# Performance work log

Measured on AMD Instinct MI355X. Metric: run time of the kernel, lower is better.

The kernel has to match this reference:

```python
import jax, jax.numpy as jnp
import numpy as np
from math import sqrt

P_DROP = 0.2  # dropout_rate

def setup_inputs() -> dict:
    key = jax.random.key(0)
    ks = jax.random.split(key, 5)
    B, Cin, H, W = 32, 128, 64, 64
    Cout, kh, kw = 256, 3, 3
    k = sqrt(1.0 / (Cin * kh * kw))  # He-style init std from module
    x = jax.random.normal(ks[0], (B, Cin, H, W), dtype=jnp.float32)
    weight = jax.random.normal(ks[1], (Cout, Cin, kh, kw), dtype=jnp.float32) * k
    bias = jax.random.normal(ks[2], (Cout,), dtype=jnp.float32) * k
    # uniforms used for torch.rand(...) > p per batch element ('w' mode draws fresh masks per sample)
    u_w = jax.random.uniform(ks[3], (B, Cout, Cin, kh, kw), dtype=jnp.float32)
    u_b = jax.random.uniform(ks[4], (B, Cout), dtype=jnp.float32)
    return {"x": x, "weight": weight, "bias": bias, "u_w": u_w, "u_b": u_b}

def reference(x, weight, bias, u_w, u_b):
    # 'w' mode: per-sample dropped-out weight/bias, conv per sample -> vmapped batched conv.
    # Note: mask is (rand > p) with NO 1/(1-p) rescaling, matching the torch code.
    w_mask = (u_w > P_DROP).astype(weight.dtype)          # [B,O,I,kh,kw]
    b_mask = (u_b > P_DROP).astype(bias.dtype)            # [B,O]
    w_per = weight[None] * w_mask                          # [B,O,I,kh,kw]
    b_per = bias[None] * b_mask                            # [B,O]

    def conv_one(xi, wi):  # xi: [Cin,H,W], wi: [O,I,kh,kw]
        return jax.lax.conv_general_dilated(
            xi[None], wi,
            window_strides=(1, 1),
            padding=((1, 1), (1, 1)),
            dimension_numbers=("NCHW", "OIHW", "NCHW"),
        )[0]

    y = jax.vmap(conv_one)(x, w_per)                       # [B,O,H,W]
    return y + b_per[:, :, None, None]
```

## Files before the change

### kernel.cpp

```cpp
#include <hip/hip_runtime.h>
#include <cstdint>
#include <cstddef>

#define CIN   128
#define COUT  256
#define HW    64
#define NSP   4096
#define KTOT  1152
#define BATCH 32
#define PDROP 0.2f
#define LDT   40

__device__ __forceinline__ unsigned short f2bf(float f) {
    unsigned int u = __builtin_bit_cast(unsigned int, f);
    u += 0x7fffu + ((u >> 16) & 1u);
    return (unsigned short)(u >> 16);
}

__device__ __align__(16) unsigned short g_zeros[64] = {0};

__device__ __forceinline__ void gl_lds16(const unsigned short* g, unsigned short* l) {
    __builtin_amdgcn_global_load_lds(
        (const __attribute__((address_space(1))) unsigned int*)g,
        (__attribute__((address_space(3))) unsigned int*)l,
        16, 0, 0);
}

__global__ __launch_bounds__(256) void prepass(
        const float* __restrict__ weight, const float* __restrict__ u_w,
        const float* __restrict__ x,
        unsigned short* __restrict__ wt, unsigned short* __restrict__ xt)
{
    __shared__ unsigned int shp[64 * 65];
    unsigned short* sh16 = reinterpret_cast<unsigned short*>(shp);
    const int t256 = threadIdx.x;

    if (blockIdx.x < 4096) {
        const int half = t256 >> 7;
        const int i    = t256 & 127;
        const int bo   = blockIdx.x * 2 + half;
        const int o    = bo & (COUT - 1);
        unsigned short* tile = sh16 + half * KTOT;
        const float* wsrc = weight + (size_t)o  * KTOT + i * 9;
        const float* usrc = u_w    + (size_t)bo * KTOT + i * 9;
        float wv9[9], uv9[9];
        #pragma unroll
        for (int r = 0; r < 9; ++r) { wv9[r] = wsrc[r]; uv9[r] = usrc[r]; }
        #pragma unroll
        for (int r = 0; r < 9; ++r)
            tile[r * CIN + i] = f2bf((uv9[r] > PDROP) ? wv9[r] : 0.f);
        __syncthreads();
        const uint4* src = reinterpret_cast<const uint4*>(tile);
        uint4* dst = reinterpret_cast<uint4*>(wt + (size_t)bo * KTOT);
        dst[i] = src[i];
        if (i < 16) dst[128 + i] = src[128 + i];
    } else {
        const int bidx = blockIdx.x - 4096;
        const int b    = bidx >> 6;
        const int hw0  = (bidx & 63) * 64;
        const int ib   = t256 >> 4;
        const int hw4  = (t256 & 15) * 4;
        #pragma unroll
        for (int j = 0; j < 4; ++j) {
            const int p = ib + 16 * j;
            const float4 v0 = *reinterpret_cast<const float4*>(
                x + ((size_t)(b * CIN + 2 * p)) * NSP + hw0 + hw4);
            const float4 v1 = *reinterpret_cast<const float4*>(
                x + ((size_t)(b * CIN + 2 * p + 1)) * NSP + hw0 + hw4);
            const float e0[4] = {v0.x, v0.y, v0.z, v0.w};
            const float e1[4] = {v1.x, v1.y, v1.z, v1.w};
            #pragma unroll
            for (int c = 0; c < 4; ++c) {
                const unsigned int val =
                    (unsigned int)f2bf(e0[c]) | ((unsigned int)f2bf(e1[c]) << 16);
                shp[(hw4 + c) * 65 + p] = val;
            }
        }
        __syncthreads();
        #pragma unroll
        for (int j = 0; j < 4; ++j) {
            const int idx  = j * 256 + t256;
            const int row  = idx >> 4;
            const int part = idx & 15;
            uint4 v;
            v.x = shp[row * 65 + part * 4 + 0];
            v.y = shp[row * 65 + part * 4 + 1];
            v.z = shp[row * 65 + part * 4 + 2];
            v.w = shp[row * 65 + part * 4 + 3];
            *reinterpret_cast<uint4*>(
                xt + ((size_t)(b * NSP + hw0 + row)) * CIN + part * 8) = v;
        }
    }
}

__global__ __launch_bounds__(256, 2) void conv_v5(
        const unsigned short* __restrict__ wt,
        const unsigned short* __restrict__ xt,
        const float* __restrict__ bias, const float* __restrict__ u_b,
        float* __restrict__ out)
{
    using frag  = __attribute__((ext_vector_type(8))) short;
    using f32x4 = __attribute__((ext_vector_type(4))) float;

    __shared__ unsigned short Xs[4 * 66 * 64];
    __shared__ unsigned short As[2][128 * 64];

    const int tid  = threadIdx.x;
    const int lane = tid & 63;
    const int q    = lane >> 4;
    const int l15  = lane & 15;
    const int wv   = tid >> 6;
    const int wm   = (wv >> 1) * 64;
    const int wn   = (wv & 1) * 64;
    const int wnrow = wn >> 6;

    const int f   = blockIdx.x + 32 * blockIdx.y + 64 * blockIdx.z;
    const int wid = (f & 7) * 256 + (f >> 3);
    const int b   = wid >> 6;
    const int m0  = ((wid >> 5) & 1) * 128;
    const int n0  = (wid & 31) * 128;
    const int ph0 = n0 >> 6;

    const unsigned short* wtb = wt + (size_t)(b * COUT + m0) * KTOT;
    const unsigned short* xtb = xt + (size_t)b * NSP * CIN;

    const int r8 = lane >> 3;
    const int p8 = lane & 7;
    const int cx = p8 ^ r8;
    const unsigned short* gA[4];
    #pragma unroll
    for (int j = 0; j < 4; ++j) {
        const int row = wv * 32 + j * 8 + r8;
        gA[j] = wtb + (size_t)row * KTOT + cx * 8;
    }

    const int kcl = (lane & 7) ^ ((1 + (lane >> 3)) & 7);
    const int xsrc_lane = (lane >> 3) * CIN + kcl * 8;
    const int hhx = ph0 - 1 + wv;
    const bool vrow = ((unsigned)hhx < 64u);
    unsigned short* const xdst = &Xs[(wv * 66 + 1) * 64];

    const int l7 = l15 & 7;
    const int physk0 = q ^ l7;
    const int physk1 = (4 + q) ^ l7;
    const int a_base = (wm + l15) * 64;
    int xoff[4];
    #pragma unroll
    for (int ni = 0; ni < 4; ++ni) xoff[ni] = (ni * 16 + l15 + 1) * 64;
    int xr[3][2];
    #pragma unroll
    for (int dxi = 0; dxi < 3; ++dxi)
        #pragma unroll
        for (int ki = 0; ki < 2; ++ki)
            xr[dxi][ki] = ((ki * 4 + q) ^ ((l15 + dxi) & 7)) * 8;

    f32x4 acc[4][4];
    #pragma unroll
    for (int i = 0; i < 4; ++i)
        #pragma unroll
        for (int j = 0; j < 4; ++j)
            acc[i][j] = (f32x4){0.f, 0.f, 0.f, 0.f};

    {
        const int cell = tid >> 5;
        const int rr   = cell >> 1;
        const int cc   = (cell & 1) ? 65 : 0;
        *reinterpret_cast<unsigned int*>(
            &Xs[(rr * 66 + cc) * 64 + (tid & 31) * 2]) = 0u;
    }

    auto stage_a = [&](int k0, int buf) {
        #pragma unroll
        for (int j = 0; j < 4; ++j)
            gl_lds16(gA[j] + k0, &As[buf][(wv * 32 + j * 8) * 64]);
    };
    auto stage_x = [&](int i0) {
        const unsigned short* sx = vrow
            ? xtb + (size_t)hhx * HW * CIN + i0 + xsrc_lane
            : g_zeros;
        #pragma unroll
        for (int g = 0; g < 8; ++g)
            gl_lds16(vrow ? (sx + g * 8 * CIN) : sx, xdst + g * 512);
    };

    stage_a(0, 0);
    stage_x(0);

    #pragma unroll
    for (int it = 0; it < 18; ++it) {
        const int tap = it % 9;
        const int cur = it & 1;

        if (it == 9) stage_x(64);

        if (it < 17) {
            const int nit = it + 1;
            stage_a((nit % 9) * 128 + (nit / 9) * 64, nit & 1);
        }

        if (it == 0)      asm volatile("s_waitcnt vmcnt(4) lgkmcnt(0)" ::: "memory");
        else if (it < 17) asm volatile("s_waitcnt vmcnt(4)" ::: "memory");
        else              asm volatile("s_waitcnt vmcnt(0)" ::: "memory");
        __builtin_amdgcn_s_barrier();

        const int dy  = tap / 3 - 1;
        const int dx  = tap - 3 * (tap / 3) - 1;
        const int dxi = dx + 1;
        const int cb  = (wnrow + dy + 1) * 4224 + dx * 64;

        __builtin_amdgcn_s_setprio(1);
        #pragma unroll
        for (int ki = 0; ki < 2; ++ki) {
            const int pk = ki ? physk1 : physk0;
            frag af[4], bfr[4];
            #pragma unroll
            for (int mi = 0; mi < 4; ++mi)
                af[mi] = *reinterpret_cast<const frag*>(
                    &As[cur][a_base + mi * 1024 + pk * 8]);
            #pragma unroll
            for (int ni = 0; ni < 4; ++ni)
                bfr[ni] = *reinterpret_cast<const frag*>(
                    &Xs[cb + xoff[ni] + xr[dxi][ki]]);
            #pragma unroll
            for (int mi = 0; mi < 4; ++mi)
                #pragma unroll
                for (int ni = 0; ni < 4; ++ni)
                    acc[mi][ni] = __builtin_amdgcn_mfma_f32_16x16x32_bf16(
                        af[mi], bfr[ni], acc[mi][ni], 0, 0, 0);
        }
        __builtin_amdgcn_s_setprio(0);

        if (it < 17) __builtin_amdgcn_s_barrier();
    }

    float* ob = out + (size_t)b * COUT * NSP;
    #pragma unroll
    for (int mi = 0; mi < 4; ++mi) {
        #pragma unroll
        for (int rg = 0; rg < 4; ++rg) {
            const int o  = m0 + wm + mi * 16 + q * 4 + rg;
            const float bvv = (u_b[b * COUT + o] > PDROP) ? bias[o] : 0.f;
            float* orow = ob + (size_t)o * NSP + n0 + wn + l15;
            #pragma unroll
            for (int ni = 0; ni < 4; ++ni)
                orow[ni * 16] = acc[mi][ni][rg] + bvv;
        }
    }
}

template<bool USE_WS>
__global__ __launch_bounds__(256) void conv_fb(
        const float* __restrict__ x, const float* __restrict__ weight,
        const float* __restrict__ bias, const float* __restrict__ u_w,
        const float* __restrict__ u_b, const unsigned short* __restrict__ wt,
        float* __restrict__ out)
{
    using frag  = __attribute__((ext_vector_type(8))) short;
    using f32x4 = __attribute__((ext_vector_type(4))) float;

    __shared__ unsigned short As[128 * LDT];
    __shared__ unsigned short Bs[128 * LDT];

    const int tid  = threadIdx.x;
    const int lane = tid & 63;
    const int q    = lane >> 4;
    const int l15  = lane & 15;
    const int wv   = tid >> 6;
    const int wm   = (wv >> 1) * 64;
    const int wn   = (wv & 1) * 64;

    const int b  = blockIdx.z;
    const int m0 = blockIdx.y * 128;
    const int n0 = blockIdx.x * 128;

    const int arow = tid >> 1;
    const int acol = (tid & 1) * 16;
    const int pn = tid & 127;
    const int kh = (tid >> 7) * 16;
    const int p  = n0 + pn;
    const int ph = p >> 6;
    const int pw = p & 63;

    const float* xb = x + (size_t)b * CIN * NSP;

    f32x4 acc[4][4];
    #pragma unroll
    for (int i = 0; i < 4; ++i)
        #pragma unroll
        for (int j = 0; j < 4; ++j)
            acc[i][j] = (f32x4){0.f, 0.f, 0.f, 0.f};

    const int a_rd = (wm + l15) * LDT + q * 8;
    const int b_rd = (wn + l15) * LDT + q * 8;

    for (int s = 0; s < 36; ++s) {
        const int r  = s >> 2;
        const int i0 = (s & 3) * 32;
        const int k0 = s * 32;

        uint4 av0, av1;
        float aw[16], au[16];
        if (USE_WS) {
            const uint4* src = reinterpret_cast<const uint4*>(
                wt + ((size_t)(b * COUT + m0 + arow)) * KTOT + k0 + acol);
            av0 = src[0];
            av1 = src[1];
        } else {
            const float* wsrc = weight + (size_t)(m0 + arow) * KTOT;
            const float* usrc = u_w + (size_t)(b * COUT + m0 + arow) * KTOT;
            #pragma unroll
            for (int ii = 0; ii < 16; ++ii) {
                const int kk = (i0 + acol + ii) * 9 + r;
                aw[ii] = wsrc[kk];
                au[ii] = usrc[kk];
            }
        }

        const int hh = ph + (r / 3) - 1;
        const int ww = pw + (r % 3) - 1;
        float bx[16];
        #pragma unroll
        for (int j = 0; j < 16; ++j) bx[j] = 0.f;
        if (((unsigned)hh < 64u) && ((unsigned)ww < 64u)) {
            const float* xsrc = xb + (size_t)(i0 + kh) * NSP + hh * HW + ww;
            #pragma unroll
            for (int j = 0; j < 16; ++j) bx[j] = xsrc[(size_t)j * NSP];
        }

        __syncthreads();

        if (USE_WS) {
            uint4* d = reinterpret_cast<uint4*>(&As[arow * LDT + acol]);
            d[0] = av0; d[1] = av1;
        } else {
            union { unsigned short u16[16]; uint4 v[2]; } tu;
            #pragma unroll
            for (int ii = 0; ii < 16; ++ii)
                tu.u16[ii] = f2bf((au[ii] > PDROP) ? aw[ii] : 0.f);
            uint4* d = reinterpret_cast<uint4*>(&As[arow * LDT + acol]);
            d[0] = tu.v[0]; d[1] = tu.v[1];
        }
        {
            union { unsigned short u16[16]; uint4 v[2]; } tu;
            #pragma unroll
            for (int j = 0; j < 16; ++j) tu.u16[j] = f2bf(bx[j]);
            uint4* d = reinterpret_cast<uint4*>(&Bs[pn * LDT + kh]);
            d[0] = tu.v[0]; d[1] = tu.v[1];
        }

        __syncthreads();

        frag af[4], bfr[4];
        #pragma unroll
        for (int mi = 0; mi < 4; ++mi)
            af[mi] = *reinterpret_cast<const frag*>(&As[a_rd + mi * 16 * LDT]);
        #pragma unroll
        for (int ni = 0; ni < 4; ++ni)
            bfr[ni] = *reinterpret_cast<const frag*>(&Bs[b_rd + ni * 16 * LDT]);
        #pragma unroll
        for (int mi = 0; mi < 4; ++mi)
            #pragma unroll
            for (int ni = 0; ni < 4; ++ni)
                acc[mi][ni] = __builtin_amdgcn_mfma_f32_16x16x32_bf16(
                    af[mi], bfr[ni], acc[mi][ni], 0, 0, 0);
    }

    float* ob = out + (size_t)b * COUT * NSP;
    #pragma unroll
    for (int mi = 0; mi < 4; ++mi) {
        #pragma unroll
        for (int rg = 0; rg < 4; ++rg) {
            const int o = m0 + wm + mi * 16 + q * 4 + rg;
            const float bvv = (u_b[b * COUT + o] > PDROP) ? bias[o] : 0.f;
            float* orow = ob + (size_t)o * NSP + n0 + wn + l15;
            #pragma unroll
            for (int ni = 0; ni < 4; ++ni)
                orow[ni * 16] = acc[mi][ni][rg] + bvv;
        }
    }
}

extern "C" void kernel_launch(void* const* d_in, const int* in_sizes, int n_in,
                              void* d_out, int out_size, void* d_ws, size_t ws_size,
                              hipStream_t stream)
{
    const float* x      = (const float*)d_in[0];
    const float* weight = (const float*)d_in[1];
    const float* bias   = (const float*)d_in[2];
    const float* u_w    = (const float*)d_in[3];
    const float* u_b    = (const float*)d_in[4];
    float* out = (float*)d_out;

    const size_t wt_bytes = (size_t)BATCH * COUT * KTOT * sizeof(unsigned short);
    const size_t xt_bytes = (size_t)BATCH * NSP * CIN * sizeof(unsigned short);
    dim3 grid(NSP / 128, COUT / 128, BATCH);

    if (ws_size >= wt_bytes + xt_bytes) {
        unsigned short* wtp = (unsigned short*)d_ws;
        unsigned short* xtp = (unsigned short*)((char*)d_ws + wt_bytes);
        prepass<<<4096 + 2048, 256, 0, stream>>>(weight, u_w, x, wtp, xtp);
        conv_v5<<<grid, 256, 0, stream>>>(wtp, xtp, bias, u_b, out);
    } else if (ws_size >= wt_bytes) {
        unsigned short* wtp = (unsigned short*)d_ws;
        prepass<<<4096, 256, 0, stream>>>(weight, u_w, x, wtp, nullptr);
        conv_fb<true><<<grid, 256, 0, stream>>>(x, weight, bias, u_w, u_b, wtp, out);
    } else {
        conv_fb<false><<<grid, 256, 0, stream>>>(x, weight, bias, u_w, u_b, nullptr, out);
    }
}
```

Baseline: 299.0 us.

## Load weight fragments directly from global into registers, dropping LDS A staging

The weight (A) operand no longer goes through a double-buffered LDS tile. Each lane now loads its MFMA fragments straight from global memory into registers, prefetching one k-step ahead, and the per-iteration barriers go away. Freeing the 32KB of A shared memory lets the launch bound rise to three blocks per SM. The cost is that each wave re-fetches weight rows from global/L2 instead of sharing them through LDS, and those loads are uncoalesced 16-byte per-lane reads whose latency is hidden only by a single-stage register prefetch.

```diff
diff --git a/kernel.cpp b/kernel.cpp
--- a/kernel.cpp
+++ b/kernel.cpp
@@ -93,7 +93,7 @@
     }
 }
 
-__global__ __launch_bounds__(256, 2) void conv_v5(
+__global__ __launch_bounds__(256, 3) void conv_v6(
         const unsigned short* __restrict__ wt,
         const unsigned short* __restrict__ xt,
         const float* __restrict__ bias, const float* __restrict__ u_b,
@@ -103,7 +103,6 @@
     using f32x4 = __attribute__((ext_vector_type(4))) float;
 
     __shared__ unsigned short Xs[4 * 66 * 64];
-    __shared__ unsigned short As[2][128 * 64];
 
     const int tid  = threadIdx.x;
     const int lane = tid & 63;
@@ -124,15 +123,11 @@
     const unsigned short* wtb = wt + (size_t)(b * COUT + m0) * KTOT;
     const unsigned short* xtb = xt + (size_t)b * NSP * CIN;
 
-    const int r8 = lane >> 3;
-    const int p8 = lane & 7;
-    const int cx = p8 ^ r8;
-    const unsigned short* gA[4];
-    #pragma unroll
-    for (int j = 0; j < 4; ++j) {
-        const int row = wv * 32 + j * 8 + r8;
-        gA[j] = wtb + (size_t)row * KTOT + cx * 8;
-    }
+    const char* gAr[4];
+    #pragma unroll
+    for (int mi = 0; mi < 4; ++mi)
+        gAr[mi] = reinterpret_cast<const char*>(
+            wtb + (size_t)(wm + mi * 16 + l15) * KTOT + q * 8);
 
     const int kcl = (lane & 7) ^ ((1 + (lane >> 3)) & 7);
     const int xsrc_lane = (lane >> 3) * CIN + kcl * 8;
@@ -140,10 +135,6 @@
     const bool vrow = ((unsigned)hhx < 64u);
     unsigned short* const xdst = &Xs[(wv * 66 + 1) * 64];
 
-    const int l7 = l15 & 7;
-    const int physk0 = q ^ l7;
-    const int physk1 = (4 + q) ^ l7;
-    const int a_base = (wm + l15) * 64;
     int xoff[4];
     #pragma unroll
     for (int ni = 0; ni < 4; ++ni) xoff[ni] = (ni * 16 + l15 + 1) * 64;
@@ -169,11 +160,6 @@
             &Xs[(rr * 66 + cc) * 64 + (tid & 31) * 2]) = 0u;
     }
 
-    auto stage_a = [&](int k0, int buf) {
-        #pragma unroll
-        for (int j = 0; j < 4; ++j)
-            gl_lds16(gA[j] + k0, &As[buf][(wv * 32 + j * 8) * 64]);
-    };
     auto stage_x = [&](int i0) {
         const unsigned short* sx = vrow
             ? xtb + (size_t)hhx * HW * CIN + i0 + xsrc_lane
@@ -183,54 +169,50 @@
             gl_lds16(vrow ? (sx + g * 8 * CIN) : sx, xdst + g * 512);
     };
 
-    stage_a(0, 0);
-    stage_x(0);
-
-    #pragma unroll
-    for (int it = 0; it < 18; ++it) {
-        const int tap = it % 9;
-        const int cur = it & 1;
-
-        if (it == 9) stage_x(64);
-
-        if (it < 17) {
-            const int nit = it + 1;
-            stage_a((nit % 9) * 128 + (nit / 9) * 64, nit & 1);
-        }
-
-        if (it == 0)      asm volatile("s_waitcnt vmcnt(4) lgkmcnt(0)" ::: "memory");
-        else if (it < 17) asm volatile("s_waitcnt vmcnt(4)" ::: "memory");
-        else              asm volatile("s_waitcnt vmcnt(0)" ::: "memory");
-        __builtin_amdgcn_s_barrier();
-
-        const int dy  = tap / 3 - 1;
-        const int dx  = tap - 3 * (tap / 3) - 1;
-        const int dxi = dx + 1;
-        const int cb  = (wnrow + dy + 1) * 4224 + dx * 64;
-
-        __builtin_amdgcn_s_setprio(1);
-        #pragma unroll
-        for (int ki = 0; ki < 2; ++ki) {
-            const int pk = ki ? physk1 : physk0;
-            frag af[4], bfr[4];
-            #pragma unroll
-            for (int mi = 0; mi < 4; ++mi)
-                af[mi] = *reinterpret_cast<const frag*>(
-                    &As[cur][a_base + mi * 1024 + pk * 8]);
+    #pragma unroll
+    for (int s2 = 0; s2 < 2; ++s2) {
+        const int i0 = s2 * 64;
+
+        if (s2) __syncthreads();
+        stage_x(i0);
+        __syncthreads();
+
+        frag afr[2][4];
+        #pragma unroll
+        for (int mi = 0; mi < 4; ++mi)
+            afr[0][mi] = *reinterpret_cast<const frag*>(gAr[mi] + (i0 * 2));
+
+        #pragma unroll
+        for (int p = 0; p < 18; ++p) {
+            const int cur = p & 1;
+            if (p + 1 < 18) {
+                const int koff = (((p + 1) >> 1) * 128 + i0 + ((p + 1) & 1) * 32) * 2;
+                #pragma unroll
+                for (int mi = 0; mi < 4; ++mi)
+                    afr[cur ^ 1][mi] = *reinterpret_cast<const frag*>(gAr[mi] + koff);
+            }
+            const int tap = p >> 1;
+            const int ki  = p & 1;
+            const int dy  = tap / 3 - 1;
+            const int dx  = tap - 3 * (tap / 3) - 1;
+            const int dxi = dx + 1;
+            const int cb  = (wnrow + dy + 1) * 4224 + dx * 64;
+
+            frag bfr[4];
             #pragma unroll
             for (int ni = 0; ni < 4; ++ni)
                 bfr[ni] = *reinterpret_cast<const frag*>(
                     &Xs[cb + xoff[ni] + xr[dxi][ki]]);
+
+            __builtin_amdgcn_s_setprio(1);
             #pragma unroll
             for (int mi = 0; mi < 4; ++mi)
                 #pragma unroll
                 for (int ni = 0; ni < 4; ++ni)
                     acc[mi][ni] = __builtin_amdgcn_mfma_f32_16x16x32_bf16(
-                        af[mi], bfr[ni], acc[mi][ni], 0, 0, 0);
-        }
-        __builtin_amdgcn_s_setprio(0);
-
-        if (it < 17) __builtin_amdgcn_s_barrier();
+                        afr[cur][mi], bfr[ni], acc[mi][ni], 0, 0, 0);
+            __builtin_amdgcn_s_setprio(0);
+        }
     }
 
     float* ob = out + (size_t)b * COUT * NSP;
@@ -399,7 +381,7 @@
         unsigned short* wtp = (unsigned short*)d_ws;
         unsigned short* xtp = (unsigned short*)((char*)d_ws + wt_bytes);
         prepass<<<4096 + 2048, 256, 0, stream>>>(weight, u_w, x, wtp, xtp);
-        conv_v5<<<grid, 256, 0, stream>>>(wtp, xtp, bias, u_b, out);
+        conv_v6<<<grid, 256, 0, stream>>>(wtp, xtp, bias, u_b, out);
     } else if (ws_size >= wt_bytes) {
         unsigned short* wtp = (unsigned short*)d_ws;
         prepass<<<4096, 256, 0, stream>>>(weight, u_w, x, wtp, nullptr);
```

Measured after the change: 352.8 us. +18.0%, slower.
